# Performance work log

Hardware: AMD Instinct MI355X
Metric: run time of the kernel (lower is better)

The kernel has to match this reference:

```python
import jax, jax.numpy as jnp
import numpy as np

# Modulated deformable conv2d (torchvision semantics): per kernel tap, sample the
# input at a runtime-offset location via bilinear interpolation (zero padding
# outside the image), modulate with mask, then do the weighted accumulation.

STRIDE = (1, 1)
PADDING = (1, 1)
DILATION = (1, 1)


def deform_conv2d(x, offset, mask, weight, bias):
    B, C, H, W = x.shape
    O, Cg, kh, kw = weight.shape
    K = kh * kw
    og = offset.shape[1] // (2 * K)          # offset groups
    Ho, Wo = offset.shape[2], offset.shape[3]
    sh, sw = STRIDE
    ph, pw = PADDING
    dh, dw = DILATION

    off = offset.reshape(B, og, K, 2, Ho, Wo)
    ki = jnp.arange(K)
    base_ky = ((ki // kw) * dh).astype(x.dtype)            # [K]
    base_kx = ((ki % kw) * dw).astype(x.dtype)
    base_h = (jnp.arange(Ho) * sh - ph).astype(x.dtype)    # [Ho]
    base_w = (jnp.arange(Wo) * sw - pw).astype(x.dtype)    # [Wo]
    # sampling positions, [B, og, K, Ho, Wo]
    p_y = off[:, :, :, 0] + base_ky[None, None, :, None, None] + base_h[None, None, None, :, None]
    p_x = off[:, :, :, 1] + base_kx[None, None, :, None, None] + base_w[None, None, None, None, :]

    y0 = jnp.floor(p_y)
    x0 = jnp.floor(p_x)
    ly = p_y - y0
    lx = p_x - x0
    y0i = y0.astype(jnp.int32)
    x0i = x0.astype(jnp.int32)

    Cog = C // og
    x_flat = x.reshape(B, og, Cog, H * W)

    def gather(yi, xi):
        valid = ((yi >= 0) & (yi < H) & (xi >= 0) & (xi < W))
        idx = jnp.clip(yi, 0, H - 1) * W + jnp.clip(xi, 0, W - 1)
        idx_flat = idx.reshape(B, og, 1, K * Ho * Wo)
        v = jnp.take_along_axis(x_flat, idx_flat, axis=3).reshape(B, og, Cog, K, Ho, Wo)
        return v * valid[:, :, None].astype(x.dtype)

    w00 = ((1 - ly) * (1 - lx))[:, :, None]
    w01 = ((1 - ly) * lx)[:, :, None]
    w10 = (ly * (1 - lx))[:, :, None]
    w11 = (ly * lx)[:, :, None]
    val = (w00 * gather(y0i, x0i) + w01 * gather(y0i, x0i + 1)
           + w10 * gather(y0i + 1, x0i) + w11 * gather(y0i + 1, x0i + 1))

    if mask is not None:
        val = val * mask.reshape(B, og, K, Ho, Wo)[:, :, None]

    # grouped conv accumulation over sampled taps
    G = C // Cg                               # conv groups (=1 here)
    val = val.reshape(B, G, C // G, K, Ho, Wo)
    w = weight.reshape(G, O // G, Cg, K)
    out = jnp.einsum('bgckhw,gock->bgohw', val, w).reshape(B, O, Ho, Wo)
    if bias is not None:
        out = out + bias[None, :, None, None]
    return out


def setup_inputs() -> dict:
    key = jax.random.key(0)
    k1, k2, k3, k4, k5 = jax.random.split(key, 5)
    B, C, H, W = 4, 64, 128, 128
    O, kh, kw = 64, 3, 3
    return {
        'input': jax.random.normal(k1, (B, C, H, W), dtype=jnp.float32),
        'offset': jax.random.normal(k2, (B, 2 * kh * kw, H, W), dtype=jnp.float32),
        'mask': jax.random.uniform(k3, (B, kh * kw, H, W), dtype=jnp.float32),
        'weight': jax.random.normal(k4, (O, C, kh, kw), dtype=jnp.float32) * (1.0 / np.sqrt(C * kh * kw)),
        'bias': jax.random.normal(k5, (O,), dtype=jnp.float32) * 0.01,
    }


def reference(input, offset, mask, weight, bias):
    return deform_conv2d(input, offset, mask, weight, bias)
```

## Files before the change

kernel.cpp:

```cpp
#include <hip/hip_runtime.h>


#define BB 4
#define CC 64
#define HH 128
#define WW 128
#define OO 64
#define KHW 3
#define KK 9
#define HW (HH * WW)

typedef __bf16 bf16_t;
typedef bf16_t bf16x8 __attribute__((ext_vector_type(8)));
typedef float f32x4 __attribute__((ext_vector_type(4)));

__global__ __launch_bounds__(256) void prep_kernel(const float* __restrict__ x,
                                                   bf16_t* __restrict__ xt,
                                                   const float* __restrict__ w,
                                                   bf16_t* __restrict__ wf) {
    __shared__ float tile[64 * 65];
    const int t = threadIdx.x;
    if (blockIdx.x < BB * 256) {
        const int b  = blockIdx.x >> 8;
        const int p0 = (blockIdx.x & 255) << 6;
#pragma unroll
        for (int i = 0; i < 16; ++i) {
            int c = i * 4 + (t >> 6);
            int p = t & 63;
            tile[c * 65 + p] = x[(b * CC + c) * HW + p0 + p];
        }
        __syncthreads();
#pragma unroll
        for (int i = 0; i < 16; ++i) {
            int p = i * 4 + (t >> 6);
            int c = t & 63;
            xt[(size_t)((b * HW) + p0 + p) * CC + c] = (bf16_t)tile[c * 65 + p];
        }
    } else {
        int i = (blockIdx.x - BB * 256) * 256 + t;
        if (i >= OO * CC * KK) return;
        int j    = i & 7;
        int lane = (i >> 3) & 63;
        int nt   = (i >> 9) & 3;
        int q    = (i >> 11) & 1;
        int k    = i >> 12;
        int o = nt * 16 + (lane & 15);
        int c = q * 32 + ((lane >> 4) << 3) + j;
        wf[i] = (bf16_t)w[(o * CC + c) * KK + k];
    }
}

__global__ __launch_bounds__(256, 4) void deform_conv_mfma(
    const bf16_t* __restrict__ xt, const float* __restrict__ offset,
    const float* __restrict__ mask, const bf16x8* __restrict__ wf,
    const float* __restrict__ bias, float* __restrict__ out) {
    const int t    = threadIdx.x;
    const int wg   = (blockIdx.x & 7) * ((BB * 256) >> 3) + (blockIdx.x >> 3);
    const int b    = wg >> 8;
    const int ti   = wg & 255;
    const int r0   = ((ti >> 4) << 3);
    const int c0   = ((ti & 15) << 3);
    const int lane = t & 63;
    const int wv   = t >> 6;
    const int col  = lane & 15;
    const int quad = lane >> 4;
    const int prow = r0 + 2 * wv + (col >> 3);
    const int pcol = c0 + (col & 7);
    const int rem  = prow * WW + pcol;
    const int wy0  = r0 - 4;
    const int wx0  = c0 - 4;
    const int cb   = quad << 3;

    __shared__ bf16_t V[256 * 64];

    const bf16_t* xb  = xt + (size_t)b * HW * CC;
    const float* offp = offset + (size_t)b * (2 * KK) * HW + rem;
    const float* mp   = mask + (size_t)b * KK * HW + rem;

    {
        const int i  = t >> 4;
        const int j  = t & 15;
        const int cy = min(max(wy0 + i, 0), HH - 1);
        const int cx = min(max(wx0 + j, 0), WW - 1);
        const bf16_t* src = xb + (size_t)(cy * WW + cx) * CC;
        bf16_t* dst = &V[(i * 16 + j) * 64];
        const int sw = (j & 7) * 8;
#pragma unroll
        for (int s = 0; s < 8; ++s)
            *(bf16x8*)(dst + ((s * 8) ^ sw)) = *(const bf16x8*)(src + s * 8);
    }
    __syncthreads();

    f32x4 acc[4];
#pragma unroll
    for (int nt = 0; nt < 4; ++nt) acc[nt] = (f32x4){0.f, 0.f, 0.f, 0.f};

    float offy = offp[0];
    float offx = offp[HW];
    float mm   = mp[0];

#pragma unroll
    for (int k = 0; k < KK; ++k) {
        float n_offy = 0.f, n_offx = 0.f, n_mm = 0.f;
        if (k < KK - 1) {
            n_offy = offp[(2 * k + 2) * HW];
            n_offx = offp[(2 * k + 3) * HW];
            n_mm   = mp[(k + 1) * HW];
        }

        float py = offy + (float)(k / KHW) + (float)(prow - 1);
        float px = offx + (float)(k % KHW) + (float)(pcol - 1);
        float fy0 = floorf(py), fx0 = floorf(px);
        float ly = py - fy0, lx = px - fx0;
        int y0 = (int)fy0, x0 = (int)fx0;
        int y1 = y0 + 1, x1 = x0 + 1;
        bool vy0 = (y0 >= 0) && (y0 < HH), vy1 = (y1 >= 0) && (y1 < HH);
        bool vx0 = (x0 >= 0) && (x0 < WW), vx1 = (x1 >= 0) && (x1 < WW);
        int cy0 = min(max(y0, 0), HH - 1), cy1 = min(max(y1, 0), HH - 1);
        int cx0 = min(max(x0, 0), WW - 1), cx1 = min(max(x1, 0), WW - 1);
        float w0 = (vy0 && vx0) ? mm * (1.0f - ly) * (1.0f - lx) : 0.0f;
        float w1 = (vy0 && vx1) ? mm * (1.0f - ly) * lx : 0.0f;
        float w2 = (vy1 && vx0) ? mm * ly * (1.0f - lx) : 0.0f;
        float w3 = (vy1 && vx1) ? mm * ly * lx : 0.0f;

        int uy0 = y0 - wy0, ux0 = x0 - wx0;
        int uy1 = uy0 + 1,  ux1 = ux0 + 1;
        bool iy0 = (unsigned)uy0 < 16u, iy1 = (unsigned)uy1 < 16u;
        bool ix0 = (unsigned)ux0 < 16u, ix1 = (unsigned)ux1 < 16u;
        int qy0 = min(max(uy0, 0), 15), qy1 = min(max(uy1, 0), 15);
        int qx0 = min(max(ux0, 0), 15), qx1 = min(max(ux1, 0), 15);
        int pa = (qy0 * 16 + qx0) * 64, pb = (qy0 * 16 + qx1) * 64;
        int pc = (qy1 * 16 + qx0) * 64, pd = (qy1 * 16 + qx1) * 64;
        int sa = (qx0 & 7), sb = (qx1 & 7);

        bf16x8 g00 = *(const bf16x8*)&V[pa + ((quad ^ sa) << 3)];
        bf16x8 h00 = *(const bf16x8*)&V[pa + (((4 + quad) ^ sa) << 3)];
        bf16x8 g01 = *(const bf16x8*)&V[pb + ((quad ^ sb) << 3)];
        bf16x8 h01 = *(const bf16x8*)&V[pb + (((4 + quad) ^ sb) << 3)];
        bf16x8 g10 = *(const bf16x8*)&V[pc + ((quad ^ sa) << 3)];
        bf16x8 h10 = *(const bf16x8*)&V[pc + (((4 + quad) ^ sa) << 3)];
        bf16x8 g11 = *(const bf16x8*)&V[pd + ((quad ^ sb) << 3)];
        bf16x8 h11 = *(const bf16x8*)&V[pd + (((4 + quad) ^ sb) << 3)];

        if (w0 != 0.0f && !(iy0 && ix0)) {
            const bf16_t* p = xb + (size_t)(cy0 * WW + cx0) * CC + cb;
            g00 = *(const bf16x8*)p; h00 = *(const bf16x8*)(p + 32);
        }
        if (w1 != 0.0f && !(iy0 && ix1)) {
            const bf16_t* p = xb + (size_t)(cy0 * WW + cx1) * CC + cb;
            g01 = *(const bf16x8*)p; h01 = *(const bf16x8*)(p + 32);
        }
        if (w2 != 0.0f && !(iy1 && ix0)) {
            const bf16_t* p = xb + (size_t)(cy1 * WW + cx0) * CC + cb;
            g10 = *(const bf16x8*)p; h10 = *(const bf16x8*)(p + 32);
        }
        if (w3 != 0.0f && !(iy1 && ix1)) {
            const bf16_t* p = xb + (size_t)(cy1 * WW + cx1) * CC + cb;
            g11 = *(const bf16x8*)p; h11 = *(const bf16x8*)(p + 32);
        }

        bf16x8 af0, af1;
#pragma unroll
        for (int i = 0; i < 8; ++i) {
            float v = w0 * (float)g00[i] + w1 * (float)g01[i] +
                      w2 * (float)g10[i] + w3 * (float)g11[i];
            af0[i] = (bf16_t)v;
        }
#pragma unroll
        for (int i = 0; i < 8; ++i) {
            float v = w0 * (float)h00[i] + w1 * (float)h01[i] +
                      w2 * (float)h10[i] + w3 * (float)h11[i];
            af1[i] = (bf16_t)v;
        }

#pragma unroll
        for (int nt = 0; nt < 4; ++nt) {
            bf16x8 bfg = wf[(k * 8 + nt) * 64 + lane];
            acc[nt] = __builtin_amdgcn_mfma_f32_16x16x32_bf16(
                af0, bfg, acc[nt], 0, 0, 0);
        }
#pragma unroll
        for (int nt = 0; nt < 4; ++nt) {
            bf16x8 bfg = wf[(k * 8 + 4 + nt) * 64 + lane];
            acc[nt] = __builtin_amdgcn_mfma_f32_16x16x32_bf16(
                af1, bfg, acc[nt], 0, 0, 0);
        }

        offy = n_offy;
        offx = n_offx;
        mm   = n_mm;
    }

#pragma unroll
    for (int nt = 0; nt < 4; ++nt) {
        int o = nt * 16 + col;
        float bv = bias[o];
        f32x4 r = acc[nt];
        r.x += bv; r.y += bv; r.z += bv; r.w += bv;
        float* dst = out + (size_t)(b * OO + o) * HW +
                     (r0 + 2 * wv + (quad >> 1)) * WW + c0 + (quad & 1) * 4;
        *(f32x4*)dst = r;
    }
}

extern "C" void kernel_launch(void* const* d_in, const int* in_sizes, int n_in,
                              void* d_out, int out_size, void* d_ws,
                              size_t ws_size, hipStream_t stream) {
    const float* x      = (const float*)d_in[0];
    const float* offset = (const float*)d_in[1];
    const float* mask   = (const float*)d_in[2];
    const float* weight = (const float*)d_in[3];
    const float* bias   = (const float*)d_in[4];
    float* out = (float*)d_out;

    bf16_t* xt  = (bf16_t*)d_ws;
    bf16_t* wfr = (bf16_t*)((char*)d_ws + (size_t)BB * HW * CC * 2);

    int nwf_blocks = (OO * CC * KK + 255) / 256;
    prep_kernel<<<BB * 256 + nwf_blocks, 256, 0, stream>>>(x, xt, weight, wfr);

    deform_conv_mfma<<<BB * (HW / 64), 256, 0, stream>>>(
        xt, offset, mask, (const bf16x8*)wfr, bias, out);
}
```

Baseline: 100.1 us.

## Drop NCHW-to-NHWC bf16 transpose pass; stage halo tile directly from fp32 input

Removes the separate prep pass that converted the whole input to channel-last bf16. The main kernel now loads its 16x16x64 halo tile straight from the fp32 NCHW input, converting and swizzling into shared memory. Out-of-tile bilinear fallbacks read 16 strided fp32 values per corner instead of two vector loads. This saves a full read and write of the input, but the tile fill becomes scalar 2-byte LDS stores with larger global reads, and fallback gathers get more expensive.

```diff
diff --git a/kernel.cpp b/kernel.cpp
--- a/kernel.cpp
+++ b/kernel.cpp
@@ -14,44 +14,22 @@
 typedef bf16_t bf16x8 __attribute__((ext_vector_type(8)));
 typedef float f32x4 __attribute__((ext_vector_type(4)));
 
-__global__ __launch_bounds__(256) void prep_kernel(const float* __restrict__ x,
-                                                   bf16_t* __restrict__ xt,
-                                                   const float* __restrict__ w,
-                                                   bf16_t* __restrict__ wf) {
-    __shared__ float tile[64 * 65];
-    const int t = threadIdx.x;
-    if (blockIdx.x < BB * 256) {
-        const int b  = blockIdx.x >> 8;
-        const int p0 = (blockIdx.x & 255) << 6;
-#pragma unroll
-        for (int i = 0; i < 16; ++i) {
-            int c = i * 4 + (t >> 6);
-            int p = t & 63;
-            tile[c * 65 + p] = x[(b * CC + c) * HW + p0 + p];
-        }
-        __syncthreads();
-#pragma unroll
-        for (int i = 0; i < 16; ++i) {
-            int p = i * 4 + (t >> 6);
-            int c = t & 63;
-            xt[(size_t)((b * HW) + p0 + p) * CC + c] = (bf16_t)tile[c * 65 + p];
-        }
-    } else {
-        int i = (blockIdx.x - BB * 256) * 256 + t;
-        if (i >= OO * CC * KK) return;
-        int j    = i & 7;
-        int lane = (i >> 3) & 63;
-        int nt   = (i >> 9) & 3;
-        int q    = (i >> 11) & 1;
-        int k    = i >> 12;
-        int o = nt * 16 + (lane & 15);
-        int c = q * 32 + ((lane >> 4) << 3) + j;
-        wf[i] = (bf16_t)w[(o * CC + c) * KK + k];
-    }
+__global__ void wfrag_kernel(const float* __restrict__ w,
+                             bf16_t* __restrict__ wf) {
+    int i = blockIdx.x * blockDim.x + threadIdx.x;
+    if (i >= OO * CC * KK) return;
+    int j    = i & 7;
+    int lane = (i >> 3) & 63;
+    int nt   = (i >> 9) & 3;
+    int q    = (i >> 11) & 1;
+    int k    = i >> 12;
+    int o = nt * 16 + (lane & 15);
+    int c = q * 32 + ((lane >> 4) << 3) + j;
+    wf[i] = (bf16_t)w[(o * CC + c) * KK + k];
 }
 
 __global__ __launch_bounds__(256, 4) void deform_conv_mfma(
-    const bf16_t* __restrict__ xt, const float* __restrict__ offset,
+    const float* __restrict__ x, const float* __restrict__ offset,
     const float* __restrict__ mask, const bf16x8* __restrict__ wf,
     const float* __restrict__ bias, float* __restrict__ out) {
     const int t    = threadIdx.x;
@@ -73,21 +51,35 @@
 
     __shared__ bf16_t V[256 * 64];
 
-    const bf16_t* xb  = xt + (size_t)b * HW * CC;
+    const float* xb   = x + (size_t)b * CC * HW;
     const float* offp = offset + (size_t)b * (2 * KK) * HW + rem;
     const float* mp   = mask + (size_t)b * KK * HW + rem;
 
     {
-        const int i  = t >> 4;
-        const int j  = t & 15;
-        const int cy = min(max(wy0 + i, 0), HH - 1);
-        const int cx = min(max(wx0 + j, 0), WW - 1);
-        const bf16_t* src = xb + (size_t)(cy * WW + cx) * CC;
-        bf16_t* dst = &V[(i * 16 + j) * 64];
-        const int sw = (j & 7) * 8;
-#pragma unroll
-        for (int s = 0; s < 8; ++s)
-            *(bf16x8*)(dst + ((s * 8) ^ sw)) = *(const bf16x8*)(src + s * 8);
+        const int c  = t >> 2;
+        const int q  = t & 3;
+        const int ck = c >> 3;
+        const int ce = c & 7;
+        const float* xc = xb + (size_t)c * HW;
+        const int jj0 = q * 4 + 0, jj1 = q * 4 + 1;
+        const int jj2 = q * 4 + 2, jj3 = q * 4 + 3;
+        const int cxa = min(max(wx0 + jj0, 0), WW - 1);
+        const int cxb = min(max(wx0 + jj1, 0), WW - 1);
+        const int cxc = min(max(wx0 + jj2, 0), WW - 1);
+        const int cxd = min(max(wx0 + jj3, 0), WW - 1);
+        const int e0 = jj0 * 64 + ((ck ^ (jj0 & 7)) << 3) + ce;
+        const int e1 = jj1 * 64 + ((ck ^ (jj1 & 7)) << 3) + ce;
+        const int e2 = jj2 * 64 + ((ck ^ (jj2 & 7)) << 3) + ce;
+        const int e3 = jj3 * 64 + ((ck ^ (jj3 & 7)) << 3) + ce;
+#pragma unroll
+        for (int r = 0; r < 16; ++r) {
+            const int cy = min(max(wy0 + r, 0), HH - 1);
+            const float* row = xc + cy * WW;
+            V[r * 1024 + e0] = (bf16_t)row[cxa];
+            V[r * 1024 + e1] = (bf16_t)row[cxb];
+            V[r * 1024 + e2] = (bf16_t)row[cxc];
+            V[r * 1024 + e3] = (bf16_t)row[cxd];
+        }
     }
     __syncthreads();
 
@@ -143,20 +135,36 @@
         bf16x8 h11 = *(const bf16x8*)&V[pd + (((4 + quad) ^ sb) << 3)];
 
         if (w0 != 0.0f && !(iy0 && ix0)) {
-            const bf16_t* p = xb + (size_t)(cy0 * WW + cx0) * CC + cb;
-            g00 = *(const bf16x8*)p; h00 = *(const bf16x8*)(p + 32);
+            const float* p = xb + (size_t)cb * HW + cy0 * WW + cx0;
+#pragma unroll
+            for (int i = 0; i < 8; ++i) {
+                g00[i] = (bf16_t)p[i * HW];
+                h00[i] = (bf16_t)p[(32 + i) * HW];
+            }
         }
         if (w1 != 0.0f && !(iy0 && ix1)) {
-            const bf16_t* p = xb + (size_t)(cy0 * WW + cx1) * CC + cb;
-            g01 = *(const bf16x8*)p; h01 = *(const bf16x8*)(p + 32);
+            const float* p = xb + (size_t)cb * HW + cy0 * WW + cx1;
+#pragma unroll
+            for (int i = 0; i < 8; ++i) {
+                g01[i] = (bf16_t)p[i * HW];
+                h01[i] = (bf16_t)p[(32 + i) * HW];
+            }
         }
         if (w2 != 0.0f && !(iy1 && ix0)) {
-            const bf16_t* p = xb + (size_t)(cy1 * WW + cx0) * CC + cb;
-            g10 = *(const bf16x8*)p; h10 = *(const bf16x8*)(p + 32);
+            const float* p = xb + (size_t)cb * HW + cy1 * WW + cx0;
+#pragma unroll
+            for (int i = 0; i < 8; ++i) {
+                g10[i] = (bf16_t)p[i * HW];
+                h10[i] = (bf16_t)p[(32 + i) * HW];
+            }
         }
         if (w3 != 0.0f && !(iy1 && ix1)) {
-            const bf16_t* p = xb + (size_t)(cy1 * WW + cx1) * CC + cb;
-            g11 = *(const bf16x8*)p; h11 = *(const bf16x8*)(p + 32);
+            const float* p = xb + (size_t)cb * HW + cy1 * WW + cx1;
+#pragma unroll
+            for (int i = 0; i < 8; ++i) {
+                g11[i] = (bf16_t)p[i * HW];
+                h11[i] = (bf16_t)p[(32 + i) * HW];
+            }
         }
 
         bf16x8 af0, af1;
@@ -213,12 +221,11 @@
     const float* bias   = (const float*)d_in[4];
     float* out = (float*)d_out;
 
-    bf16_t* xt  = (bf16_t*)d_ws;
-    bf16_t* wfr = (bf16_t*)((char*)d_ws + (size_t)BB * HW * CC * 2);
-
-    int nwf_blocks = (OO * CC * KK + 255) / 256;
-    prep_kernel<<<BB * 256 + nwf_blocks, 256, 0, stream>>>(x, xt, weight, wfr);
+    bf16_t* wfr = (bf16_t*)d_ws;
+
+    int nw = OO * CC * KK;
+    wfrag_kernel<<<(nw + 255) / 256, 256, 0, stream>>>(weight, wfr);
 
     deform_conv_mfma<<<BB * (HW / 64), 256, 0, stream>>>(
-        xt, offset, mask, (const bf16x8*)wfr, bias, out);
+        x, offset, mask, (const bf16x8*)wfr, bias, out);
 }
```

After: 122.3 us. +22.2%, slower.

## Vectorize transpose stores, change LDS swizzle to row+col, raise occupancy hint

Applied to the files above, without the earlier changes.

The prep transpose now has each thread build two bf16x8 vectors from the shared tile and write them with 16-byte stores, replacing scalar 2-byte stores. The LDS swizzle key in the main kernel becomes (row+col)&7 instead of col&7, which spreads bilinear neighbors from different rows across banks and is meant to cut LDS bank conflicts. The launch-bounds minimum-blocks hint rises from 4 to 5, which may squeeze registers and cause spills.

```diff
diff --git a/kernel.cpp b/kernel.cpp
--- a/kernel.cpp
+++ b/kernel.cpp
@@ -30,12 +30,17 @@
             tile[c * 65 + p] = x[(b * CC + c) * HW + p0 + p];
         }
         __syncthreads();
-#pragma unroll
-        for (int i = 0; i < 16; ++i) {
-            int p = i * 4 + (t >> 6);
-            int c = t & 63;
-            xt[(size_t)((b * HW) + p0 + p) * CC + c] = (bf16_t)tile[c * 65 + p];
-        }
+        const int p = t >> 2;
+        const int q = t & 3;
+        bf16x8 v0, v1;
+#pragma unroll
+        for (int e = 0; e < 8; ++e) v0[e] = (bf16_t)tile[(q * 8 + e) * 65 + p];
+#pragma unroll
+        for (int e = 0; e < 8; ++e)
+            v1[e] = (bf16_t)tile[((q + 4) * 8 + e) * 65 + p];
+        bf16_t* dst = xt + (size_t)((b * HW) + p0 + p) * CC;
+        *(bf16x8*)(dst + q * 8) = v0;
+        *(bf16x8*)(dst + (q + 4) * 8) = v1;
     } else {
         int i = (blockIdx.x - BB * 256) * 256 + t;
         if (i >= OO * CC * KK) return;
@@ -50,7 +55,7 @@
     }
 }
 
-__global__ __launch_bounds__(256, 4) void deform_conv_mfma(
+__global__ __launch_bounds__(256, 5) void deform_conv_mfma(
     const bf16_t* __restrict__ xt, const float* __restrict__ offset,
     const float* __restrict__ mask, const bf16x8* __restrict__ wf,
     const float* __restrict__ bias, float* __restrict__ out) {
@@ -84,7 +89,7 @@
         const int cx = min(max(wx0 + j, 0), WW - 1);
         const bf16_t* src = xb + (size_t)(cy * WW + cx) * CC;
         bf16_t* dst = &V[(i * 16 + j) * 64];
-        const int sw = (j & 7) * 8;
+        const int sw = ((i + j) & 7) * 8;
 #pragma unroll
         for (int s = 0; s < 8; ++s)
             *(bf16x8*)(dst + ((s * 8) ^ sw)) = *(const bf16x8*)(src + s * 8);
@@ -131,16 +136,17 @@
         int qx0 = min(max(ux0, 0), 15), qx1 = min(max(ux1, 0), 15);
         int pa = (qy0 * 16 + qx0) * 64, pb = (qy0 * 16 + qx1) * 64;
         int pc = (qy1 * 16 + qx0) * 64, pd = (qy1 * 16 + qx1) * 64;
-        int sa = (qx0 & 7), sb = (qx1 & 7);
-
-        bf16x8 g00 = *(const bf16x8*)&V[pa + ((quad ^ sa) << 3)];
-        bf16x8 h00 = *(const bf16x8*)&V[pa + (((4 + quad) ^ sa) << 3)];
-        bf16x8 g01 = *(const bf16x8*)&V[pb + ((quad ^ sb) << 3)];
-        bf16x8 h01 = *(const bf16x8*)&V[pb + (((4 + quad) ^ sb) << 3)];
-        bf16x8 g10 = *(const bf16x8*)&V[pc + ((quad ^ sa) << 3)];
-        bf16x8 h10 = *(const bf16x8*)&V[pc + (((4 + quad) ^ sa) << 3)];
-        bf16x8 g11 = *(const bf16x8*)&V[pd + ((quad ^ sb) << 3)];
-        bf16x8 h11 = *(const bf16x8*)&V[pd + (((4 + quad) ^ sb) << 3)];
+        int k00 = (qx0 + qy0) & 7, k01 = (qx1 + qy0) & 7;
+        int k10 = (qx0 + qy1) & 7, k11 = (qx1 + qy1) & 7;
+
+        bf16x8 g00 = *(const bf16x8*)&V[pa + ((quad ^ k00) << 3)];
+        bf16x8 h00 = *(const bf16x8*)&V[pa + (((4 + quad) ^ k00) << 3)];
+        bf16x8 g01 = *(const bf16x8*)&V[pb + ((quad ^ k01) << 3)];
+        bf16x8 h01 = *(const bf16x8*)&V[pb + (((4 + quad) ^ k01) << 3)];
+        bf16x8 g10 = *(const bf16x8*)&V[pc + ((quad ^ k10) << 3)];
+        bf16x8 h10 = *(const bf16x8*)&V[pc + (((4 + quad) ^ k10) << 3)];
+        bf16x8 g11 = *(const bf16x8*)&V[pd + ((quad ^ k11) << 3)];
+        bf16x8 h11 = *(const bf16x8*)&V[pd + (((4 + quad) ^ k11) << 3)];
 
         if (w0 != 0.0f && !(iy0 && ix0)) {
             const bf16_t* p = xb + (size_t)(cy0 * WW + cx0) * CC + cb;
```

New measurement: 103.4 us. 1.03x slower.
